# Optimization experiments

Hardware: AMD Instinct MI355X
Metric: run time of the kernel (lower is better)

Reference implementation:

```python
import jax, jax.numpy as jnp
import numpy as np

HIDDEN = 1024
HEADS = 16
HEAD_DIM = HIDDEN // HEADS
EPS = 1e-5


def _layernorm(x, w, b):
    mu = jnp.mean(x, axis=-1, keepdims=True)
    var = jnp.mean(jnp.square(x - mu), axis=-1, keepdims=True)
    return (x - mu) * jax.lax.rsqrt(var + EPS) * w + b


def setup_inputs() -> dict:
    key = jax.random.key(0)
    ks = jax.random.split(key, 8)
    D = HIDDEN
    x = jax.random.normal(ks[0], (4, 4096, D), dtype=jnp.float32)
    s = 0.02
    return {
        "x": x,
        "qkv_w": jax.random.normal(ks[1], (3 * D, D), jnp.float32) * s,
        "qkv_b": jnp.zeros((3 * D,), jnp.float32),
        "proj_w": jax.random.normal(ks[2], (D, D), jnp.float32) * s,
        "proj_b": jnp.zeros((D,), jnp.float32),
        "ln1_w": jnp.ones((D,), jnp.float32),
        "ln1_b": jnp.zeros((D,), jnp.float32),
        "ln2_w": jnp.ones((D,), jnp.float32),
        "ln2_b": jnp.zeros((D,), jnp.float32),
        "mlp_w1": jax.random.normal(ks[3], (4 * D, D), jnp.float32) * s,
        "mlp_b1": jnp.zeros((4 * D,), jnp.float32),
        "mlp_w2": jax.random.normal(ks[4], (D, 4 * D), jnp.float32) * s,
        "mlp_b2": jnp.zeros((D,), jnp.float32),
    }


def reference(x, qkv_w, qkv_b, proj_w, proj_b, ln1_w, ln1_b, ln2_w, ln2_b,
              mlp_w1, mlp_b1, mlp_w2, mlp_b2):
    B, L, D = x.shape
    h = _layernorm(x, ln1_w, ln1_b)
    qkv = (h @ qkv_w.T + qkv_b).reshape(B, L, 3, HEADS, HEAD_DIM)
    q, k, v = qkv[:, :, 0], qkv[:, :, 1], qkv[:, :, 2]  # (B, L, H, hd)
    # NOTE: faithful to source - NO (L,H) transpose, so attention mixes
    # across the head axis per token: scores shape (B, L, H, H).
    attn = jnp.einsum('blhd,blgd->blhg', q, k) / np.sqrt(HEAD_DIM).astype(np.float32)
    attn = jax.nn.softmax(attn, axis=-1)
    out = jnp.einsum('blhg,blgd->blhd', attn, v).reshape(B, L, D)
    out = out @ proj_w.T + proj_b
    x = x + out
    h2 = _layernorm(x, ln2_w, ln2_b)
    mlp = jax.nn.gelu(h2 @ mlp_w1.T + mlp_b1, approximate=False) @ mlp_w2.T + mlp_b2
    return x + mlp
```

## Files before the change

kernel.cpp:

```cpp
#include <hip/hip_runtime.h>
#include <cstdint>
#include <cmath>


#define NTOK   16384
#define DMODEL 1024

typedef __bf16 bf16x8 __attribute__((ext_vector_type(8)));
typedef float  f32x4  __attribute__((ext_vector_type(4)));

__device__ __forceinline__ unsigned short f2bf(float f) {
    unsigned int u = __builtin_bit_cast(unsigned int, f);
    u += 0x7fffu + ((u >> 16) & 1u);
    return (unsigned short)(u >> 16);
}
__device__ __forceinline__ float bf2f(unsigned short s) {
    unsigned int u = ((unsigned int)s) << 16;
    return __builtin_bit_cast(float, u);
}

__global__ __launch_bounds__(256) void cast_f32_bf16(
    const float4* __restrict__ in, ushort4* __restrict__ out, int n4) {
    int i = blockIdx.x * 256 + threadIdx.x;
    if (i < n4) {
        float4 v = in[i];
        ushort4 o;
        o.x = f2bf(v.x); o.y = f2bf(v.y); o.z = f2bf(v.z); o.w = f2bf(v.w);
        out[i] = o;
    }
}

__global__ __launch_bounds__(256) void ln_cast(
    const float* __restrict__ x, const float* __restrict__ w,
    const float* __restrict__ b, unsigned short* __restrict__ out) {
    int tok = blockIdx.x;
    int t   = threadIdx.x;
    float4 v = ((const float4*)x)[tok * 256 + t];
    float s  = v.x + v.y + v.z + v.w;
    float ss = v.x * v.x + v.y * v.y + v.z * v.z + v.w * v.w;
    #pragma unroll
    for (int off = 32; off > 0; off >>= 1) {
        s  += __shfl_down(s, off);
        ss += __shfl_down(ss, off);
    }
    __shared__ float red[8];
    int wave = t >> 6;
    if ((t & 63) == 0) { red[wave * 2] = s; red[wave * 2 + 1] = ss; }
    __syncthreads();
    s  = red[0] + red[2] + red[4] + red[6];
    ss = red[1] + red[3] + red[5] + red[7];
    float mu  = s * (1.0f / 1024.0f);
    float var = ss * (1.0f / 1024.0f) - mu * mu;
    float rs  = rsqrtf(var + 1e-5f);
    float4 wv = ((const float4*)w)[t];
    float4 bv = ((const float4*)b)[t];
    ushort4 o;
    o.x = f2bf((v.x - mu) * rs * wv.x + bv.x);
    o.y = f2bf((v.y - mu) * rs * wv.y + bv.y);
    o.z = f2bf((v.z - mu) * rs * wv.z + bv.z);
    o.w = f2bf((v.w - mu) * rs * wv.w + bv.w);
    ((ushort4*)out)[tok * 256 + t] = o;
}

__global__ __launch_bounds__(256) void attn_heads(
    const unsigned short* __restrict__ qkv, unsigned short* __restrict__ out) {
    __shared__ float sQ[1024], sK[1024], sV[1024];
    __shared__ float sS[256];
    int tok = blockIdx.x;
    int t   = threadIdx.x;
    const unsigned short* base = qkv + (size_t)tok * 3072;
    for (int i = t; i < 1024; i += 256) {
        sQ[i] = bf2f(base[i]);
        sK[i] = bf2f(base[1024 + i]);
        sV[i] = bf2f(base[2048 + i]);
    }
    __syncthreads();
    {
        int h = t >> 4, g = t & 15;
        float s = 0.0f;
        #pragma unroll
        for (int d = 0; d < 64; ++d) s += sQ[h * 64 + d] * sK[g * 64 + d];
        sS[h * 16 + g] = s * 0.125f;
    }
    __syncthreads();
    if (t < 16) {
        float mx = -1e30f;
        for (int g = 0; g < 16; ++g) mx = fmaxf(mx, sS[t * 16 + g]);
        float sum = 0.0f;
        for (int g = 0; g < 16; ++g) {
            float e = expf(sS[t * 16 + g] - mx);
            sS[t * 16 + g] = e;
            sum += e;
        }
        float inv = 1.0f / sum;
        for (int g = 0; g < 16; ++g) sS[t * 16 + g] *= inv;
    }
    __syncthreads();
    #pragma unroll
    for (int j = 0; j < 4; ++j) {
        int o = t + 256 * j;
        int h = o >> 6, d = o & 63;
        float s = 0.0f;
        #pragma unroll
        for (int g = 0; g < 16; ++g) s += sS[h * 16 + g] * sV[g * 64 + d];
        out[(size_t)tok * 1024 + o] = f2bf(s);
    }
}

#define BM 128
#define BN 128
#define BK 32
#define LDST 40

template <int EPI>
__global__ __launch_bounds__(256) void gemm_bf16(
    const unsigned short* __restrict__ A, const unsigned short* __restrict__ W,
    const float* __restrict__ bias, const float* resid, void* Cout,
    int M, int N, int K) {
    __shared__ __align__(16) unsigned short As[BM * LDST];
    __shared__ __align__(16) unsigned short Bs[BN * LDST];

    const int t    = threadIdx.x;
    const int lane = t & 63;
    const int wave = t >> 6;
    const int wm   = wave >> 1;
    const int wn   = wave & 1;
    const int m0   = blockIdx.y * BM;
    const int n0   = blockIdx.x * BN;

    const int rowA0 = t >> 2,          colA0 = (t & 3) * 8;
    const int rowA1 = (t + 256) >> 2,  colA1 = colA0;

    const int fr = lane & 15;
    const int fq = lane >> 4;

    f32x4 acc[4][4] = {};

    for (int k0 = 0; k0 < K; k0 += BK) {
        uint4 a0 = *(const uint4*)(A + (size_t)(m0 + rowA0) * K + k0 + colA0);
        uint4 a1 = *(const uint4*)(A + (size_t)(m0 + rowA1) * K + k0 + colA1);
        uint4 b0 = *(const uint4*)(W + (size_t)(n0 + rowA0) * K + k0 + colA0);
        uint4 b1 = *(const uint4*)(W + (size_t)(n0 + rowA1) * K + k0 + colA1);
        __syncthreads();
        *(uint4*)(As + rowA0 * LDST + colA0) = a0;
        *(uint4*)(As + rowA1 * LDST + colA1) = a1;
        *(uint4*)(Bs + rowA0 * LDST + colA0) = b0;
        *(uint4*)(Bs + rowA1 * LDST + colA1) = b1;
        __syncthreads();

        bf16x8 af[4], bf[4];
        #pragma unroll
        for (int i = 0; i < 4; ++i)
            af[i] = *(const bf16x8*)(As + (wm * 64 + i * 16 + fr) * LDST + fq * 8);
        #pragma unroll
        for (int i = 0; i < 4; ++i)
            bf[i] = *(const bf16x8*)(Bs + (wn * 64 + i * 16 + fr) * LDST + fq * 8);
        #pragma unroll
        for (int im = 0; im < 4; ++im)
            #pragma unroll
            for (int in = 0; in < 4; ++in)
                acc[im][in] = __builtin_amdgcn_mfma_f32_16x16x32_bf16(
                    af[im], bf[in], acc[im][in], 0, 0, 0);
    }

    #pragma unroll
    for (int in = 0; in < 4; ++in) {
        int col = n0 + wn * 64 + in * 16 + fr;
        float bv = bias[col];
        #pragma unroll
        for (int im = 0; im < 4; ++im) {
            int rowb = m0 + wm * 64 + im * 16 + fq * 4;
            #pragma unroll
            for (int e = 0; e < 4; ++e) {
                size_t idx = (size_t)(rowb + e) * N + col;
                float v = acc[im][in][e] + bv;
                if (EPI == 0) {
                    ((unsigned short*)Cout)[idx] = f2bf(v);
                } else if (EPI == 1) {
                    ((float*)Cout)[idx] = v + resid[idx];
                } else {
                    float g = 0.5f * v * (1.0f + erff(v * 0.70710678118654752f));
                    ((unsigned short*)Cout)[idx] = f2bf(g);
                }
            }
        }
    }
}

extern "C" void kernel_launch(void* const* d_in, const int* in_sizes, int n_in,
                              void* d_out, int out_size, void* d_ws, size_t ws_size,
                              hipStream_t stream) {
    const float* x      = (const float*)d_in[0];
    const float* qkv_w  = (const float*)d_in[1];
    const float* qkv_b  = (const float*)d_in[2];
    const float* proj_w = (const float*)d_in[3];
    const float* proj_b = (const float*)d_in[4];
    const float* ln1_w  = (const float*)d_in[5];
    const float* ln1_b  = (const float*)d_in[6];
    const float* ln2_w  = (const float*)d_in[7];
    const float* ln2_b  = (const float*)d_in[8];
    const float* mlp_w1 = (const float*)d_in[9];
    const float* mlp_b1 = (const float*)d_in[10];
    const float* mlp_w2 = (const float*)d_in[11];
    const float* mlp_b2 = (const float*)d_in[12];
    float* out = (float*)d_out;

    const size_t WB = 25165824;
    char* ws = (char*)d_ws;
    unsigned short* w_qkv  = (unsigned short*)(ws);
    unsigned short* w_proj = (unsigned short*)(ws + 6291456);
    unsigned short* w_m1   = (unsigned short*)(ws + 8388608);
    unsigned short* w_m2   = (unsigned short*)(ws + 16777216);

    int T = NTOK;
    while (T >= 256 && WB + (size_t)T * 12288 > ws_size) T >>= 1;
    if (T < 256) {
        hipMemcpyAsync(out, x, (size_t)NTOK * DMODEL * sizeof(float),
                       hipMemcpyDeviceToDevice, stream);
        return;
    }

    unsigned short* hbuf = (unsigned short*)(ws + WB);
    unsigned short* abuf = (unsigned short*)(ws + WB + (size_t)T * 2048);
    unsigned short* qmbuf= (unsigned short*)(ws + WB + (size_t)T * 4096);

    cast_f32_bf16<<<3072, 256, 0, stream>>>((const float4*)qkv_w,  (ushort4*)w_qkv,  786432);
    cast_f32_bf16<<<1024, 256, 0, stream>>>((const float4*)proj_w, (ushort4*)w_proj, 262144);
    cast_f32_bf16<<<4096, 256, 0, stream>>>((const float4*)mlp_w1, (ushort4*)w_m1,   1048576);
    cast_f32_bf16<<<4096, 256, 0, stream>>>((const float4*)mlp_w2, (ushort4*)w_m2,   1048576);

    for (int tok0 = 0; tok0 < NTOK; tok0 += T) {
        const float* xc   = x   + (size_t)tok0 * DMODEL;
        float*       outc = out + (size_t)tok0 * DMODEL;

        ln_cast<<<T, 256, 0, stream>>>(xc, ln1_w, ln1_b, hbuf);
        gemm_bf16<0><<<dim3(3072 / BN, T / BM), 256, 0, stream>>>(
            hbuf, w_qkv, qkv_b, nullptr, qmbuf, T, 3072, 1024);
        attn_heads<<<T, 256, 0, stream>>>(qmbuf, abuf);
        gemm_bf16<1><<<dim3(1024 / BN, T / BM), 256, 0, stream>>>(
            abuf, w_proj, proj_b, xc, (void*)outc, T, 1024, 1024);
        ln_cast<<<T, 256, 0, stream>>>(outc, ln2_w, ln2_b, hbuf);
        gemm_bf16<2><<<dim3(4096 / BN, T / BM), 256, 0, stream>>>(
            hbuf, w_m1, mlp_b1, nullptr, qmbuf, T, 4096, 1024);
        gemm_bf16<1><<<dim3(1024 / BN, T / BM), 256, 0, stream>>>(
            qmbuf, w_m2, mlp_b2, outc, (void*)outc, T, 1024, 4096);
    }
}
```

Measured before the change: 1.071 ms.

## Use direct global-to-LDS loads with XOR swizzle and XCD-aware block mapping in GEMM

```diff
diff --git a/kernel.cpp b/kernel.cpp
--- a/kernel.cpp
+++ b/kernel.cpp
@@ -8,6 +8,8 @@
 
 typedef __bf16 bf16x8 __attribute__((ext_vector_type(8)));
 typedef float  f32x4  __attribute__((ext_vector_type(4)));
+typedef unsigned int __attribute__((address_space(1))) as1_uint;
+typedef unsigned int __attribute__((address_space(3))) as3_uint;
 
 __device__ __forceinline__ unsigned short f2bf(float f) {
     unsigned int u = __builtin_bit_cast(unsigned int, f);
@@ -17,6 +19,10 @@
 __device__ __forceinline__ float bf2f(unsigned short s) {
     unsigned int u = ((unsigned int)s) << 16;
     return __builtin_bit_cast(float, u);
+}
+
+__device__ __forceinline__ void g2l16(const unsigned short* g, unsigned short* l) {
+    __builtin_amdgcn_global_load_lds((const as1_uint*)g, (as3_uint*)l, 16, 0, 0);
 }
 
 __global__ __launch_bounds__(256) void cast_f32_bf16(
@@ -110,51 +116,65 @@
 #define BM 128
 #define BN 128
 #define BK 32
-#define LDST 40
 
 template <int EPI>
 __global__ __launch_bounds__(256) void gemm_bf16(
     const unsigned short* __restrict__ A, const unsigned short* __restrict__ W,
     const float* __restrict__ bias, const float* resid, void* Cout,
     int M, int N, int K) {
-    __shared__ __align__(16) unsigned short As[BM * LDST];
-    __shared__ __align__(16) unsigned short Bs[BN * LDST];
+    __shared__ __align__(16) unsigned short As[BM * BK];
+    __shared__ __align__(16) unsigned short Bs[BN * BK];
 
     const int t    = threadIdx.x;
     const int lane = t & 63;
     const int wave = t >> 6;
     const int wm   = wave >> 1;
     const int wn   = wave & 1;
-    const int m0   = blockIdx.y * BM;
-    const int n0   = blockIdx.x * BN;
-
-    const int rowA0 = t >> 2,          colA0 = (t & 3) * 8;
-    const int rowA1 = (t + 256) >> 2,  colA1 = colA0;
-
-    const int fr = lane & 15;
-    const int fq = lane >> 4;
+
+    const int nx  = N >> 7;
+    const int nx8 = nx >> 3;
+    const int bid = blockIdx.x;
+    const int xcd = bid & 7;
+    const int lid = bid >> 3;
+    const int mloc = lid / nx8;
+    const int nloc = lid - mloc * nx8;
+    const int m0 = mloc << 7;
+    const int n0 = (xcd * nx8 + nloc) << 7;
+
+    const int rS0   = wave * 16 + (lane >> 2);
+    const int rS1   = rS0 + 64;
+    const int cpos  = lane & 3;
+    const int cg    = cpos ^ ((rS0 >> 1) & 3);
+    const unsigned short* gA0 = A + (size_t)(m0 + rS0) * K + cg * 8;
+    const unsigned short* gA1 = A + (size_t)(m0 + rS1) * K + cg * 8;
+    const unsigned short* gB0 = W + (size_t)(n0 + rS0) * K + cg * 8;
+    const unsigned short* gB1 = W + (size_t)(n0 + rS1) * K + cg * 8;
+    unsigned short* lA0 = As + wave * 512;
+    unsigned short* lA1 = As + 2048 + wave * 512;
+    unsigned short* lB0 = Bs + wave * 512;
+    unsigned short* lB1 = Bs + 2048 + wave * 512;
+
+    const int fr  = lane & 15;
+    const int fq  = lane >> 4;
+    const int csw = fq ^ ((fr >> 1) & 3);
 
     f32x4 acc[4][4] = {};
 
     for (int k0 = 0; k0 < K; k0 += BK) {
-        uint4 a0 = *(const uint4*)(A + (size_t)(m0 + rowA0) * K + k0 + colA0);
-        uint4 a1 = *(const uint4*)(A + (size_t)(m0 + rowA1) * K + k0 + colA1);
-        uint4 b0 = *(const uint4*)(W + (size_t)(n0 + rowA0) * K + k0 + colA0);
-        uint4 b1 = *(const uint4*)(W + (size_t)(n0 + rowA1) * K + k0 + colA1);
         __syncthreads();
-        *(uint4*)(As + rowA0 * LDST + colA0) = a0;
-        *(uint4*)(As + rowA1 * LDST + colA1) = a1;
-        *(uint4*)(Bs + rowA0 * LDST + colA0) = b0;
-        *(uint4*)(Bs + rowA1 * LDST + colA1) = b1;
+        g2l16(gA0 + k0, lA0);
+        g2l16(gA1 + k0, lA1);
+        g2l16(gB0 + k0, lB0);
+        g2l16(gB1 + k0, lB1);
         __syncthreads();
 
         bf16x8 af[4], bf[4];
         #pragma unroll
         for (int i = 0; i < 4; ++i)
-            af[i] = *(const bf16x8*)(As + (wm * 64 + i * 16 + fr) * LDST + fq * 8);
+            af[i] = *(const bf16x8*)(As + (wm * 64 + i * 16 + fr) * 32 + csw * 8);
         #pragma unroll
         for (int i = 0; i < 4; ++i)
-            bf[i] = *(const bf16x8*)(Bs + (wn * 64 + i * 16 + fr) * LDST + fq * 8);
+            bf[i] = *(const bf16x8*)(Bs + (wn * 64 + i * 16 + fr) * 32 + csw * 8);
         #pragma unroll
         for (int im = 0; im < 4; ++im)
             #pragma unroll
@@ -232,17 +252,18 @@
     for (int tok0 = 0; tok0 < NTOK; tok0 += T) {
         const float* xc   = x   + (size_t)tok0 * DMODEL;
         float*       outc = out + (size_t)tok0 * DMODEL;
+        const int my = T / BM;
 
         ln_cast<<<T, 256, 0, stream>>>(xc, ln1_w, ln1_b, hbuf);
-        gemm_bf16<0><<<dim3(3072 / BN, T / BM), 256, 0, stream>>>(
+        gemm_bf16<0><<<(3072 / BN) * my, 256, 0, stream>>>(
             hbuf, w_qkv, qkv_b, nullptr, qmbuf, T, 3072, 1024);
         attn_heads<<<T, 256, 0, stream>>>(qmbuf, abuf);
-        gemm_bf16<1><<<dim3(1024 / BN, T / BM), 256, 0, stream>>>(
+        gemm_bf16<1><<<(1024 / BN) * my, 256, 0, stream>>>(
             abuf, w_proj, proj_b, xc, (void*)outc, T, 1024, 1024);
         ln_cast<<<T, 256, 0, stream>>>(outc, ln2_w, ln2_b, hbuf);
-        gemm_bf16<2><<<dim3(4096 / BN, T / BM), 256, 0, stream>>>(
+        gemm_bf16<2><<<(4096 / BN) * my, 256, 0, stream>>>(
             hbuf, w_m1, mlp_b1, nullptr, qmbuf, T, 4096, 1024);
-        gemm_bf16<1><<<dim3(1024 / BN, T / BM), 256, 0, stream>>>(
+        gemm_bf16<1><<<(1024 / BN) * my, 256, 0, stream>>>(
             qmbuf, w_m2, mlp_b2, outc, (void*)outc, T, 1024, 4096);
     }
 }
```

Result: faster. 1.050 ms (-2.0%).
